# Performance work log

Hardware: AMD Instinct MI355X
Metric: run time of the kernel (lower is better)

## Reference

```python
import jax, jax.numpy as jnp
import numpy as np

T, B, N, H = 512, 256, 64, 64  # timepoints, batch, INPUT_SIZE neurons, hidden_size_LSTM


def setup_inputs() -> dict:
    key = jax.random.key(0)
    ks = jax.random.split(key, 12)
    s = 0.1
    inp = {
        "input": jax.random.normal(ks[0], (T, B, N), dtype=jnp.float32),
        # per-neuron Linear(1,10): weight [N,10,1], bias [N,10]
        "w1": jax.random.normal(ks[1], (N, 10, 1), dtype=jnp.float32) * s,
        "b1": jax.random.normal(ks[2], (N, 10), dtype=jnp.float32) * s,
        # per-neuron Linear(10,1): weight [N,1,10], bias [N,1]
        "w2": jax.random.normal(ks[3], (N, 1, 10), dtype=jnp.float32) * s,
        "b2": jax.random.normal(ks[4], (N, 1), dtype=jnp.float32) * s,
        # shared LSTMCell(1, H): torch layout [4H,1],[4H,H],[4H],[4H] (i,f,g,o)
        "W_ih": jax.random.normal(ks[5], (4 * H, 1), dtype=jnp.float32) * s,
        "W_hh": jax.random.normal(ks[6], (4 * H, H), dtype=jnp.float32) * s,
        "b_ih": jax.random.normal(ks[7], (4 * H,), dtype=jnp.float32) * s,
        "b_hh": jax.random.normal(ks[8], (4 * H,), dtype=jnp.float32) * s,
        # shared linearLSTM(H,1): weight [1,H], bias [1]
        "wg": jax.random.normal(ks[9], (1, H), dtype=jnp.float32) * s,
        "bg": jax.random.normal(ks[10], (1,), dtype=jnp.float32) * s,
    }
    return inp


def reference(input, w1, b1, w2, b2, W_ih, W_hh, b_ih, b_hh, wg, bg):
    Tn, Bn, Nn = input.shape
    Hn = W_hh.shape[1]
    dt = input.dtype

    # Per-neuron input2hidden / hidden2out linears, vectorized over (t, b, n).
    outHid = input[..., None] * w1[:, :, 0] + b1              # [T,B,N,10]
    outLin = jnp.einsum("tbnh,nh->tbn", outHid, w2[:, 0, :]) + b2[:, 0]  # [T,B,N]

    def step(carry, x_t):
        h, c = carry                                          # each [B,N,H]
        gates = (x_t[..., None] * W_ih[:, 0] + b_ih
                 + jnp.einsum("bnh,gh->bng", h, W_hh) + b_hh)  # [B,N,4H]
        i_g, f_g, g_g, o_g = jnp.split(gates, 4, axis=-1)
        i_g = jax.nn.sigmoid(i_g)
        f_g = jax.nn.sigmoid(f_g)
        g_g = jnp.tanh(g_g)
        o_g = jax.nn.sigmoid(o_g)
        c = f_g * c + i_g * g_g
        h = o_g * jnp.tanh(c)
        g_t = h @ wg[0] + bg[0]                               # [B,N]
        return (h, c), g_t

    h0 = jnp.zeros((Bn, Nn, Hn), dtype=dt)
    c0 = jnp.zeros((Bn, Nn, Hn), dtype=dt)
    (_, _), gs = jax.lax.scan(step, (h0, c0), outLin)          # gs: [T,B,N]

    # Original code: g list starts as [1]; g_t appended BEFORE reading g[i-1].
    # i=0 -> g[-1] = g_0 (current); i=1 -> g[0] = 1; i>=2 -> g[i-1] = g_{i-2}.
    ones_row = jnp.ones((1, Bn, Nn), dtype=dt)
    g_prev = jnp.concatenate([gs[:1], ones_row, gs[: Tn - 2]], axis=0)  # [T,B,N]

    output = g_prev * jax.nn.softplus(outLin - 1.0)            # log(1+exp(outLin-1))
    return output
```

## Files before the change

kernel.cpp:

```cpp
#include <hip/hip_runtime.h>
#include <hip/hip_bf16.h>

#define TT 512
#define MCELLS 16384
#define LOG2E 1.44269504088896340736f
#define LN2   0.69314718055994530942f

typedef __attribute__((ext_vector_type(8))) short bf16x8;
typedef __attribute__((ext_vector_type(4))) float f32x4;
typedef __attribute__((ext_vector_type(4))) unsigned u32x4;

__device__ __forceinline__ short f2bf(float f) {
    __hip_bfloat16 h = __float2bfloat16(f);
    return __builtin_bit_cast(short, h);
}
__device__ __forceinline__ unsigned cvtpk(float a, float b) {
    unsigned r;
    asm("v_cvt_pk_bf16_f32 %0, %1, %2" : "=v"(r) : "v"(a), "v"(b));
    return r;
}

__global__ __launch_bounds__(256, 4)
void lstm_net_kernel(const float* __restrict__ input,
                     const float* __restrict__ w1,
                     const float* __restrict__ b1,
                     const float* __restrict__ w2,
                     const float* __restrict__ b2,
                     const float* __restrict__ W_ih,
                     const float* __restrict__ W_hh,
                     const float* __restrict__ b_ih,
                     const float* __restrict__ b_hh,
                     const float* __restrict__ wg,
                     const float* __restrict__ bg,
                     float* __restrict__ out)
{
    __shared__ float tanY[2049];
    __shared__ float tanD[2049];
    __shared__ __align__(16) char hbuf[2 * 16 * 144];

    const int tid  = threadIdx.x;
    const int wv   = tid >> 6;
    const int lane = tid & 63;
    const int lo   = lane & 15;
    const int hi   = lane >> 4;

    for (int idx = tid; idx < 2049; idx += 256) {
        const float xv = (float)idx * 0.0078125f - 8.0f;
        const float e0 = __builtin_amdgcn_exp2f(2.0f * LOG2E * xv);
        const float e1 = __builtin_amdgcn_exp2f(2.0f * LOG2E * (xv + 0.0078125f));
        const float t0 = 1.0f - 2.0f / (1.0f + e0);
        const float t1 = 1.0f - 2.0f / (1.0f + e1);
        tanY[idx] = t0;
        tanD[idx] = t1 - t0;
    }

    for (int o = tid; o < (2 * 16 * 144) / 4; o += 256)
        ((unsigned*)hbuf)[o] = 0u;

    const int cell = blockIdx.x * 16 + lo;
    const int n    = cell & 63;
    float a_n = 0.f, c_n = 0.f;
    #pragma unroll
    for (int k = 0; k < 10; ++k) {
        a_n += w1[n * 10 + k] * w2[n * 10 + k];
        c_n += b1[n * 10 + k] * w2[n * 10 + k];
    }
    c_n += b2[n];
    const float bgv = bg[0];

    bf16x8 AWf[4][3];
    #pragma unroll
    for (int g = 0; g < 4; ++g) {
        const int row = (g * 4 + wv) * 16 + lo;
        #pragma unroll
        for (int kk = 0; kk < 2; ++kk) {
            const float* src = W_hh + row * 64 + kk * 32 + hi * 8;
            bf16x8 v;
            #pragma unroll
            for (int e = 0; e < 8; ++e) v[e] = f2bf(src[e]);
            AWf[g][kk] = v;
        }
        bf16x8 vx = {};
        if (hi == 0) {
            vx[0] = f2bf(W_ih[row]);
            vx[1] = f2bf(b_ih[row] + b_hh[row]);
        }
        AWf[g][2] = vx;
    }
    bf16x8 AWg[2];
    #pragma unroll
    for (int kk = 0; kk < 2; ++kk) {
        bf16x8 v = {};
        if (lo == 0) {
            const float* src = wg + kk * 32 + hi * 8;
            #pragma unroll
            for (int e = 0; e < 8; ++e) v[e] = f2bf(src[e]);
        }
        AWg[kk] = v;
    }

    const f32x4 zero4 = {0.f, 0.f, 0.f, 0.f};
    f32x4 cst = zero4;
    float sp0 = 0.f;
    float gA  = 0.f;
    const float* inP  = input + cell;
    float*       outP = out + cell;
    float raw_next = inP[0];

    __syncthreads();

    for (int t = 0; t < TT; ++t) {
        const float raw = raw_next;
        raw_next = inP[((t + 1) & (TT - 1)) * MCELLS];
        const float x = raw * a_n + c_n;

        u32x4 bxi = {0u, 0u, 0u, 0u};
        bxi[0] = (hi == 0) ? cvtpk(x, 1.0f) : 0u;
        const bf16x8 bx = __builtin_bit_cast(bf16x8, bxi);

        const char* hrd = hbuf + (t & 1) * 2304 + lo * 144;
        const bf16x8 bf0 = *(const bf16x8*)(hrd + hi * 16);
        const bf16x8 bf1 = *(const bf16x8*)(hrd + 64 + hi * 16);

        f32x4 acc[4];
        #pragma unroll
        for (int g = 0; g < 4; ++g) {
            acc[g] = __builtin_amdgcn_mfma_f32_16x16x32_bf16(AWf[g][2], bx,  zero4, 0, 0, 0);
            acc[g] = __builtin_amdgcn_mfma_f32_16x16x32_bf16(AWf[g][0], bf0, acc[g], 0, 0, 0);
            acc[g] = __builtin_amdgcn_mfma_f32_16x16x32_bf16(AWf[g][1], bf1, acc[g], 0, 0, 0);
        }
        f32x4 accg;
        accg = __builtin_amdgcn_mfma_f32_16x16x32_bf16(AWg[0], bf0, zero4, 0, 0, 0);
        accg = __builtin_amdgcn_mfma_f32_16x16x32_bf16(AWg[1], bf1, accg, 0, 0, 0);

        float hv[4];
        #pragma unroll
        for (int r = 0; r < 4; ++r) {
            const float ip = acc[0][r];
            const float fp = acc[1][r];
            const float gp = acc[2][r];
            const float op = acc[3][r];

            const float Ei = __builtin_amdgcn_exp2f(-LOG2E * ip);
            const float Ef = __builtin_amdgcn_exp2f(-LOG2E * fp);
            const float Eo = __builtin_amdgcn_exp2f(-LOG2E * op);

            const float gcl = __builtin_amdgcn_fmed3f(gp, -8.0f, 7.9921875f);
            const float gu  = fmaf(gcl, 128.0f, 1024.0f);
            const int   gi  = (int)gu;
            const float gfr = gu - (float)gi;
            const float tg  = fmaf(gfr, tanD[gi], tanY[gi]);

            const float A1 = 1.f + Ei;
            const float A2 = 1.f + Ef;
            const float cp = (cst[r] * A1 + tg * A2) *
                             __builtin_amdgcn_rcpf(A1 * A2);
            cst[r] = cp;

            const float ccl = __builtin_amdgcn_fmed3f(cp, -8.0f, 7.9921875f);
            const float cu  = fmaf(ccl, 128.0f, 1024.0f);
            const int   ci  = (int)cu;
            const float cfr = cu - (float)ci;
            const float tc  = fmaf(cfr, tanD[ci], tanY[ci]);

            hv[r] = tc * __builtin_amdgcn_rcpf(1.f + Eo);
        }
        uint2 pk;
        pk.x = cvtpk(hv[0], hv[1]);
        pk.y = cvtpk(hv[2], hv[3]);
        *(uint2*)(hbuf + ((t + 1) & 1) * 2304 + lo * 144 + wv * 32 + hi * 8) = pk;

        if (((t == 0) ? (wv == 1) : ((t & 3) == wv)) && hi == 0) {
            const float spE = __builtin_amdgcn_exp2f(LOG2E * (x - 1.f));
            const float sp  = LN2 * __builtin_amdgcn_logf(1.f + spE);
            if (t == 0) {
                sp0 = sp;
            } else if (t == 1) {
                outP[MCELLS] = sp;
                outP[0] = (accg[0] + bgv) * sp0;
            } else {
                outP[t * MCELLS] = (gA + bgv) * sp;
            }
        }
        gA = accg[0];
        __syncthreads();
    }
}

extern "C" void kernel_launch(void* const* d_in, const int* in_sizes, int n_in,
                              void* d_out, int out_size, void* d_ws, size_t ws_size,
                              hipStream_t stream) {
    const float* input = (const float*)d_in[0];
    const float* w1    = (const float*)d_in[1];
    const float* b1    = (const float*)d_in[2];
    const float* w2    = (const float*)d_in[3];
    const float* b2    = (const float*)d_in[4];
    const float* W_ih  = (const float*)d_in[5];
    const float* W_hh  = (const float*)d_in[6];
    const float* b_ih  = (const float*)d_in[7];
    const float* b_hh  = (const float*)d_in[8];
    const float* wg    = (const float*)d_in[9];
    const float* bg    = (const float*)d_in[10];

    lstm_net_kernel<<<dim3(1024), dim3(256), 0, stream>>>(
        input, w1, b1, w2, b2, W_ih, W_hh, b_ih, b_hh, wg, bg, (float*)d_out);
}
```

Measured before the change: 710.0 us.

## Split gate work across eight waves with interleaved gate rows per MFMA tile

Raises the block from 4 to 8 waves, so each wave computes two MFMA tiles instead of four. W_hh rows are permuted so each accumulator's four outputs are the i,f,g,o gates of one hidden unit. Each lane then updates one cell per tile and writes a single bf16 h value to LDS. The aim is to shorten the per-step serial critical path by spreading the sequential recurrence across more waves. The cost is more waves per barrier, scalar 2-byte LDS stores, and higher register and occupancy pressure.

Result: slower. 1.010 ms (+42.2%).

```diff
diff --git a/kernel.cpp b/kernel.cpp
--- a/kernel.cpp
+++ b/kernel.cpp
@@ -20,7 +20,14 @@
     return r;
 }
 
-__global__ __launch_bounds__(256, 4)
+#define LUT_TANH(xv, dst) {                                            \
+    const float _c = __builtin_amdgcn_fmed3f((xv), -8.0f, 7.9921875f); \
+    const float _u = fmaf(_c, 128.0f, 1024.0f);                        \
+    const int   _i = (int)_u;                                          \
+    const float _f = _u - (float)_i;                                   \
+    (dst) = fmaf(_f, tanD[_i], tanY[_i]); }
+
+__global__ __launch_bounds__(512, 8)
 void lstm_net_kernel(const float* __restrict__ input,
                      const float* __restrict__ w1,
                      const float* __restrict__ b1,
@@ -44,7 +51,7 @@
     const int lo   = lane & 15;
     const int hi   = lane >> 4;
 
-    for (int idx = tid; idx < 2049; idx += 256) {
+    for (int idx = tid; idx < 2049; idx += 512) {
         const float xv = (float)idx * 0.0078125f - 8.0f;
         const float e0 = __builtin_amdgcn_exp2f(2.0f * LOG2E * xv);
         const float e1 = __builtin_amdgcn_exp2f(2.0f * LOG2E * (xv + 0.0078125f));
@@ -54,7 +61,7 @@
         tanD[idx] = t1 - t0;
     }
 
-    for (int o = tid; o < (2 * 16 * 144) / 4; o += 256)
+    for (int o = tid; o < (2 * 16 * 144) / 4; o += 512)
         ((unsigned*)hbuf)[o] = 0u;
 
     const int cell = blockIdx.x * 16 + lo;
@@ -68,24 +75,25 @@
     c_n += b2[n];
     const float bgv = bg[0];
 
-    bf16x8 AWf[4][3];
+    bf16x8 AWf[2][3];
     #pragma unroll
-    for (int g = 0; g < 4; ++g) {
-        const int row = (g * 4 + wv) * 16 + lo;
+    for (int t2 = 0; t2 < 2; ++t2) {
+        const int T    = 2 * wv + t2;
+        const int Wrow = (lo & 3) * 64 + 4 * T + (lo >> 2);
         #pragma unroll
         for (int kk = 0; kk < 2; ++kk) {
-            const float* src = W_hh + row * 64 + kk * 32 + hi * 8;
+            const float* src = W_hh + Wrow * 64 + kk * 32 + hi * 8;
             bf16x8 v;
             #pragma unroll
             for (int e = 0; e < 8; ++e) v[e] = f2bf(src[e]);
-            AWf[g][kk] = v;
+            AWf[t2][kk] = v;
         }
         bf16x8 vx = {};
         if (hi == 0) {
-            vx[0] = f2bf(W_ih[row]);
-            vx[1] = f2bf(b_ih[row] + b_hh[row]);
-        }
-        AWf[g][2] = vx;
+            vx[0] = f2bf(W_ih[Wrow]);
+            vx[1] = f2bf(b_ih[Wrow] + b_hh[Wrow]);
+        }
+        AWf[t2][2] = vx;
     }
     bf16x8 AWg[2];
     #pragma unroll
@@ -100,7 +108,7 @@
     }
 
     const f32x4 zero4 = {0.f, 0.f, 0.f, 0.f};
-    f32x4 cst = zero4;
+    float cst[2] = {0.f, 0.f};
     float sp0 = 0.f;
     float gA  = 0.f;
     const float* inP  = input + cell;
@@ -122,55 +130,46 @@
         const bf16x8 bf0 = *(const bf16x8*)(hrd + hi * 16);
         const bf16x8 bf1 = *(const bf16x8*)(hrd + 64 + hi * 16);
 
-        f32x4 acc[4];
+        f32x4 acc[2];
         #pragma unroll
-        for (int g = 0; g < 4; ++g) {
-            acc[g] = __builtin_amdgcn_mfma_f32_16x16x32_bf16(AWf[g][2], bx,  zero4, 0, 0, 0);
-            acc[g] = __builtin_amdgcn_mfma_f32_16x16x32_bf16(AWf[g][0], bf0, acc[g], 0, 0, 0);
-            acc[g] = __builtin_amdgcn_mfma_f32_16x16x32_bf16(AWf[g][1], bf1, acc[g], 0, 0, 0);
+        for (int t2 = 0; t2 < 2; ++t2) {
+            acc[t2] = __builtin_amdgcn_mfma_f32_16x16x32_bf16(AWf[t2][2], bx,  zero4,  0, 0, 0);
+            acc[t2] = __builtin_amdgcn_mfma_f32_16x16x32_bf16(AWf[t2][0], bf0, acc[t2], 0, 0, 0);
+            acc[t2] = __builtin_amdgcn_mfma_f32_16x16x32_bf16(AWf[t2][1], bf1, acc[t2], 0, 0, 0);
         }
         f32x4 accg;
         accg = __builtin_amdgcn_mfma_f32_16x16x32_bf16(AWg[0], bf0, zero4, 0, 0, 0);
         accg = __builtin_amdgcn_mfma_f32_16x16x32_bf16(AWg[1], bf1, accg, 0, 0, 0);
 
-        float hv[4];
+        char* hw = hbuf + ((t + 1) & 1) * 2304 + lo * 144;
         #pragma unroll
-        for (int r = 0; r < 4; ++r) {
-            const float ip = acc[0][r];
-            const float fp = acc[1][r];
-            const float gp = acc[2][r];
-            const float op = acc[3][r];
+        for (int t2 = 0; t2 < 2; ++t2) {
+            const float ip = acc[t2][0];
+            const float fp = acc[t2][1];
+            const float gp = acc[t2][2];
+            const float op = acc[t2][3];
 
             const float Ei = __builtin_amdgcn_exp2f(-LOG2E * ip);
             const float Ef = __builtin_amdgcn_exp2f(-LOG2E * fp);
             const float Eo = __builtin_amdgcn_exp2f(-LOG2E * op);
 
-            const float gcl = __builtin_amdgcn_fmed3f(gp, -8.0f, 7.9921875f);
-            const float gu  = fmaf(gcl, 128.0f, 1024.0f);
-            const int   gi  = (int)gu;
-            const float gfr = gu - (float)gi;
-            const float tg  = fmaf(gfr, tanD[gi], tanY[gi]);
+            float tg;
+            LUT_TANH(gp, tg);
 
             const float A1 = 1.f + Ei;
             const float A2 = 1.f + Ef;
-            const float cp = (cst[r] * A1 + tg * A2) *
+            const float cp = (cst[t2] * A1 + tg * A2) *
                              __builtin_amdgcn_rcpf(A1 * A2);
-            cst[r] = cp;
-
-            const float ccl = __builtin_amdgcn_fmed3f(cp, -8.0f, 7.9921875f);
-            const float cu  = fmaf(ccl, 128.0f, 1024.0f);
-            const int   ci  = (int)cu;
-            const float cfr = cu - (float)ci;
-            const float tc  = fmaf(cfr, tanD[ci], tanY[ci]);
-
-            hv[r] = tc * __builtin_amdgcn_rcpf(1.f + Eo);
-        }
-        uint2 pk;
-        pk.x = cvtpk(hv[0], hv[1]);
-        pk.y = cvtpk(hv[2], hv[3]);
-        *(uint2*)(hbuf + ((t + 1) & 1) * 2304 + lo * 144 + wv * 32 + hi * 8) = pk;
-
-        if (((t == 0) ? (wv == 1) : ((t & 3) == wv)) && hi == 0) {
+            cst[t2] = cp;
+
+            float tc;
+            LUT_TANH(cp, tc);
+            const float hv = tc * __builtin_amdgcn_rcpf(1.f + Eo);
+
+            *(short*)(hw + 2 * (8 * wv + 4 * t2 + hi)) = f2bf(hv);
+        }
+
+        if (((t == 0) ? (wv == 1) : ((t & 7) == wv)) && hi == 0) {
             const float spE = __builtin_amdgcn_exp2f(LOG2E * (x - 1.f));
             const float sp  = LN2 * __builtin_amdgcn_logf(1.f + spE);
             if (t == 0) {
@@ -202,6 +201,6 @@
     const float* wg    = (const float*)d_in[9];
     const float* bg    = (const float*)d_in[10];
 
-    lstm_net_kernel<<<dim3(1024), dim3(256), 0, stream>>>(
+    lstm_net_kernel<<<dim3(1024), dim3(512), 0, stream>>>(
         input, w1, b1, w2, b2, W_ih, W_hh, b_ih, b_hh, wg, bg, (float*)d_out);
 }
```

## Fold input/bias into MFMA accumulator init, gate output MFMA per wave, share reciprocal

Applied to the files above, without the earlier changes.

Drops the third MFMA per gate that applied W_ih*x + bias through a padded bf16 operand. Instead the accumulator is seeded with an fp32 FMA using per-row W_ih/bias values staged in LDS, which also removes the bf16 rounding on those terms. The output-projection MFMA now runs only in the wave that writes the output at that step. The two reciprocals in the cell update are merged into one, adding a few multiplies and extra LDS reads.

Result: slower. 779.7 us (+9.8%).

```diff
diff --git a/kernel.cpp b/kernel.cpp
--- a/kernel.cpp
+++ b/kernel.cpp
@@ -8,7 +8,6 @@
 
 typedef __attribute__((ext_vector_type(8))) short bf16x8;
 typedef __attribute__((ext_vector_type(4))) float f32x4;
-typedef __attribute__((ext_vector_type(4))) unsigned u32x4;
 
 __device__ __forceinline__ short f2bf(float f) {
     __hip_bfloat16 h = __float2bfloat16(f);
@@ -19,6 +18,13 @@
     asm("v_cvt_pk_bf16_f32 %0, %1, %2" : "=v"(r) : "v"(a), "v"(b));
     return r;
 }
+
+#define LUT_TANH(xv, dst) {                                            \
+    const float _c = __builtin_amdgcn_fmed3f((xv), -8.0f, 7.9921875f); \
+    const float _u = fmaf(_c, 128.0f, 1024.0f);                        \
+    const int   _i = (int)_u;                                          \
+    const float _f = _u - (float)_i;                                   \
+    (dst) = fmaf(_f, tanD[_i], tanY[_i]); }
 
 __global__ __launch_bounds__(256, 4)
 void lstm_net_kernel(const float* __restrict__ input,
@@ -36,6 +42,7 @@
 {
     __shared__ float tanY[2049];
     __shared__ float tanD[2049];
+    __shared__ __align__(16) float2 wib[256];
     __shared__ __align__(16) char hbuf[2 * 16 * 144];
 
     const int tid  = threadIdx.x;
@@ -53,6 +60,9 @@
         tanY[idx] = t0;
         tanD[idx] = t1 - t0;
     }
+    if (tid < 256) {
+        wib[tid] = make_float2(W_ih[tid], b_ih[tid] + b_hh[tid]);
+    }
 
     for (int o = tid; o < (2 * 16 * 144) / 4; o += 256)
         ((unsigned*)hbuf)[o] = 0u;
@@ -68,7 +78,7 @@
     c_n += b2[n];
     const float bgv = bg[0];
 
-    bf16x8 AWf[4][3];
+    bf16x8 AWf[4][2];
     #pragma unroll
     for (int g = 0; g < 4; ++g) {
         const int row = (g * 4 + wv) * 16 + lo;
@@ -80,12 +90,6 @@
             for (int e = 0; e < 8; ++e) v[e] = f2bf(src[e]);
             AWf[g][kk] = v;
         }
-        bf16x8 vx = {};
-        if (hi == 0) {
-            vx[0] = f2bf(W_ih[row]);
-            vx[1] = f2bf(b_ih[row] + b_hh[row]);
-        }
-        AWf[g][2] = vx;
     }
     bf16x8 AWg[2];
     #pragma unroll
@@ -114,24 +118,31 @@
         raw_next = inP[((t + 1) & (TT - 1)) * MCELLS];
         const float x = raw * a_n + c_n;
 
-        u32x4 bxi = {0u, 0u, 0u, 0u};
-        bxi[0] = (hi == 0) ? cvtpk(x, 1.0f) : 0u;
-        const bf16x8 bx = __builtin_bit_cast(bf16x8, bxi);
-
         const char* hrd = hbuf + (t & 1) * 2304 + lo * 144;
         const bf16x8 bf0 = *(const bf16x8*)(hrd + hi * 16);
         const bf16x8 bf1 = *(const bf16x8*)(hrd + 64 + hi * 16);
 
+        if ((((t + 1) & 3) == wv) || (t == 1 && wv == 1)) {
+            f32x4 accg;
+            accg = __builtin_amdgcn_mfma_f32_16x16x32_bf16(AWg[0], bf0, zero4, 0, 0, 0);
+            accg = __builtin_amdgcn_mfma_f32_16x16x32_bf16(AWg[1], bf1, accg, 0, 0, 0);
+            gA = accg[0];
+        }
+
         f32x4 acc[4];
         #pragma unroll
         for (int g = 0; g < 4; ++g) {
-            acc[g] = __builtin_amdgcn_mfma_f32_16x16x32_bf16(AWf[g][2], bx,  zero4, 0, 0, 0);
-            acc[g] = __builtin_amdgcn_mfma_f32_16x16x32_bf16(AWf[g][0], bf0, acc[g], 0, 0, 0);
-            acc[g] = __builtin_amdgcn_mfma_f32_16x16x32_bf16(AWf[g][1], bf1, acc[g], 0, 0, 0);
-        }
-        f32x4 accg;
-        accg = __builtin_amdgcn_mfma_f32_16x16x32_bf16(AWg[0], bf0, zero4, 0, 0, 0);
-        accg = __builtin_amdgcn_mfma_f32_16x16x32_bf16(AWg[1], bf1, accg, 0, 0, 0);
+            const int base = g * 64 + wv * 16 + hi * 4;
+            const f32x4 p01 = *(const f32x4*)&wib[base];
+            const f32x4 p23 = *(const f32x4*)&wib[base + 2];
+            f32x4 ai;
+            ai[0] = fmaf(x, p01[0], p01[1]);
+            ai[1] = fmaf(x, p01[2], p01[3]);
+            ai[2] = fmaf(x, p23[0], p23[1]);
+            ai[3] = fmaf(x, p23[2], p23[3]);
+            ai = __builtin_amdgcn_mfma_f32_16x16x32_bf16(AWf[g][0], bf0, ai, 0, 0, 0);
+            acc[g] = __builtin_amdgcn_mfma_f32_16x16x32_bf16(AWf[g][1], bf1, ai, 0, 0, 0);
+        }
 
         float hv[4];
         #pragma unroll
@@ -145,25 +156,20 @@
             const float Ef = __builtin_amdgcn_exp2f(-LOG2E * fp);
             const float Eo = __builtin_amdgcn_exp2f(-LOG2E * op);
 
-            const float gcl = __builtin_amdgcn_fmed3f(gp, -8.0f, 7.9921875f);
-            const float gu  = fmaf(gcl, 128.0f, 1024.0f);
-            const int   gi  = (int)gu;
-            const float gfr = gu - (float)gi;
-            const float tg  = fmaf(gfr, tanD[gi], tanY[gi]);
-
-            const float A1 = 1.f + Ei;
-            const float A2 = 1.f + Ef;
-            const float cp = (cst[r] * A1 + tg * A2) *
-                             __builtin_amdgcn_rcpf(A1 * A2);
+            float tg;
+            LUT_TANH(gp, tg);
+
+            const float A1  = 1.f + Ei;
+            const float A2  = 1.f + Ef;
+            const float Od  = 1.f + Eo;
+            const float A12 = A1 * A2;
+            const float R   = __builtin_amdgcn_rcpf(A12 * Od);
+            const float cp  = (cst[r] * A1 + tg * A2) * (Od * R);
             cst[r] = cp;
 
-            const float ccl = __builtin_amdgcn_fmed3f(cp, -8.0f, 7.9921875f);
-            const float cu  = fmaf(ccl, 128.0f, 1024.0f);
-            const int   ci  = (int)cu;
-            const float cfr = cu - (float)ci;
-            const float tc  = fmaf(cfr, tanD[ci], tanY[ci]);
-
-            hv[r] = tc * __builtin_amdgcn_rcpf(1.f + Eo);
+            float tc;
+            LUT_TANH(cp, tc);
+            hv[r] = tc * (A12 * R);
         }
         uint2 pk;
         pk.x = cvtpk(hv[0], hv[1]);
@@ -177,12 +183,11 @@
                 sp0 = sp;
             } else if (t == 1) {
                 outP[MCELLS] = sp;
-                outP[0] = (accg[0] + bgv) * sp0;
+                outP[0] = (gA + bgv) * sp0;
             } else {
                 outP[t * MCELLS] = (gA + bgv) * sp;
             }
         }
-        gA = accg[0];
         __syncthreads();
     }
 }
```
